# Optimization experiments

Hardware: AMD Instinct MI355X
Metric: run time of the kernel (lower is better)

Reference implementation:

```python
import jax, jax.numpy as jnp
import numpy as np

H, HD = 8, 64  # num_heads, head_dim
EPS = 1e-6

def rmsnorm(x, scale):
    return x * jax.lax.rsqrt(jnp.mean(x * x, axis=-1, keepdims=True) + EPS) * scale

def lecun(key, shape):
    fan_in = shape[0]
    return jax.random.normal(key, shape, dtype=jnp.float32) * (fan_in ** -0.5)

def setup_inputs() -> dict:
    key = jax.random.key(0)
    ks = jax.random.split(key, 12)
    B, S, D = 2, 512, 512
    hidden = H * HD            # 512
    ffn = 4 * D                # 2048
    return {
        "inputs": jax.random.normal(ks[0], (B, S, D), dtype=jnp.float32),
        "mask": jnp.zeros((B, S), dtype=jnp.float32),
        "carry": jnp.zeros((B, H, HD, HD), dtype=jnp.float32),
        "ln1": jnp.ones((D,), dtype=jnp.float32),
        "Wq": lecun(ks[1], (D, hidden)),
        "Wk": lecun(ks[2], (D, hidden)),
        "Wv": lecun(ks[3], (D, hidden)),
        "attn_ln": jnp.ones((hidden,), dtype=jnp.float32),
        "Wo": lecun(ks[4], (hidden, D)),
        "bo": jnp.zeros((D,), dtype=jnp.float32),
        "ln2": jnp.ones((D,), dtype=jnp.float32),
        "Wg": lecun(ks[5], (D, ffn)),
        "Wu": lecun(ks[6], (D, ffn)),
        "Wd": lecun(ks[7], (ffn, D)),
    }

def reference(inputs, mask, carry, ln1, Wq, Wk, Wv, attn_ln, Wo, bo, ln2, Wg, Wu, Wd):
    B, S, D = inputs.shape
    skip = inputs
    x = rmsnorm(inputs, ln1)
    # projections + relu feature map
    q = jax.nn.relu((x @ Wq).reshape(B, S, H, HD))
    k = jax.nn.relu((x @ Wk).reshape(B, S, H, HD))
    v = (x @ Wv).reshape(B, S, H, HD)
    # matrix-valued state update: Bmat_t = v_t k_t^T  [B,S,H,HD,HD]
    Bmat = v[..., :, None] * k[..., None, :]
    # decay: identity, zeroed where mask==1 (episode reset)
    m = mask[:, :, None, None, None]
    A = jnp.broadcast_to(jnp.eye(HD, dtype=x.dtype), Bmat.shape) * (1.0 - m)

    def binop(lhs, rhs):
        a_i, b_i = lhs
        a_j, b_j = rhs
        return jnp.matmul(a_i, a_j), jnp.matmul(b_i, a_j) + b_j

    cum_decay, hidden_states = jax.lax.associative_scan(binop, (A, Bmat), axis=1)
    # fold in incoming carry
    states = jnp.matmul(carry[:, None], cum_decay) + hidden_states  # [B,S,H,HD,HD]
    attn = jnp.matmul(states, q[..., None]).squeeze(-1).reshape(B, S, H * HD)
    attn = rmsnorm(attn, attn_ln)
    y = attn @ Wo + bo
    final_carry = states[:, -1]
    # residual + SwiGLU FFN
    x = y + skip
    skip2 = x
    x = rmsnorm(x, ln2)
    x = (jax.nn.silu(x @ Wg) * (x @ Wu)) @ Wd
    return (final_carry, x + skip2)
```

## Files before the change

kernel.cpp:

```cpp
#include <hip/hip_runtime.h>
#include <math.h>

typedef __bf16 bf16x8 __attribute__((ext_vector_type(8)));
typedef float  f32x4  __attribute__((ext_vector_type(4)));

constexpr int B_=2, S_=512, D_=512, H_=8, HD_=64, FFN_=2048, NC_=8;
constexpr float EPS_=1e-6f;

__device__ __forceinline__ __bf16 f2bf(float f){
    union{float f;unsigned u;}x; x.f=f;
    unsigned r=(x.u+0x7fffu+((x.u>>16)&1u))>>16;
    union{unsigned short s;__bf16 b;}y; y.s=(unsigned short)r; return y.b;
}
__device__ __forceinline__ float bf2f(unsigned short s){
    union{unsigned u;float f;}x; x.u=((unsigned)s)<<16; return x.f;
}
__device__ __forceinline__ void bf8_f32(uint4 p, float* o){
    unsigned w[4]={p.x,p.y,p.z,p.w};
#pragma unroll
    for(int i=0;i<4;i++){ o[2*i]=bf2f((unsigned short)(w[i]&0xffffu)); o[2*i+1]=bf2f((unsigned short)(w[i]>>16)); }
}
__device__ __forceinline__ f32x4 MF(bf16x8 a, bf16x8 b, f32x4 c){
    return __builtin_amdgcn_mfma_f32_16x16x32_bf16(a,b,c,0,0,0);
}
#define GLOAD16(g,l) __builtin_amdgcn_global_load_lds((__attribute__((address_space(1))) const void*)(g),(__attribute__((address_space(3))) void*)(l),16,0,0)

__device__ __forceinline__ void rowsq_atomic(float* accb, int row0, int lane, float p[4]){
#pragma unroll
    for(int r=0;r<4;r++){
        float v = p[r];
        v += __shfl_xor(v, 1, 64);
        v += __shfl_xor(v, 2, 64);
        v += __shfl_xor(v, 4, 64);
        v += __shfl_xor(v, 8, 64);
        if((lane&15)==0) atomicAdd(accb + row0 + r, v);
    }
}

__global__ __launch_bounds__(256) void prep_k(const float* __restrict__ Wg,
    const float* __restrict__ Wu, const float* __restrict__ Wd,
    const float* __restrict__ Wq, const float* __restrict__ Wk,
    const float* __restrict__ Wv, const float* __restrict__ Wo,
    __bf16* __restrict__ WT, const float* __restrict__ inputs,
    float* __restrict__ rs1, float* __restrict__ rs2acc, float* __restrict__ rs3acc){
    __shared__ __bf16 s[64][72];
    int t = blockIdx.x, tid = threadIdx.x;
    if(t >= 1024){
        int row = (t-1024)*4 + (tid>>6), lane = tid&63;
        const float4* p = (const float4*)(inputs + (size_t)row*D_) + lane*2;
        float4 a=p[0], b=p[1];
        float ss = a.x*a.x+a.y*a.y+a.z*a.z+a.w*a.w + b.x*b.x+b.y*b.y+b.z*b.z+b.w*b.w;
        for(int off=32; off>0; off>>=1) ss += __shfl_down(ss, off, 64);
        if(lane==0) rs1[row] = rsqrtf(ss/(float)D_ + EPS_);
        float4 z = {0.f,0.f,0.f,0.f};
        if(t==1024) ((float4*)rs2acc)[tid] = z;
        if(t==1025) ((float4*)rs3acc)[tid] = z;
        return;
    }
    const float* src; __bf16* dst; int K,N,lt;
    if      (t<256){ src=Wg; dst=WT;          K=512;  N=2048; lt=t; }
    else if (t<512){ src=Wu; dst=WT+1048576;  K=512;  N=2048; lt=t-256; }
    else if (t<768){ src=Wd; dst=WT+2097152;  K=2048; N=512;  lt=t-512; }
    else if (t<832){ src=Wq; dst=WT+3145728;  K=512;  N=512;  lt=t-768; }
    else if (t<896){ src=Wk; dst=WT+3407872;  K=512;  N=512;  lt=t-832; }
    else if (t<960){ src=Wv; dst=WT+3670016;  K=512;  N=512;  lt=t-896; }
    else           { src=Wo; dst=WT+3932160;  K=512;  N=512;  lt=t-960; }
    int nt64 = N>>6, tk = lt/nt64, tn = lt%nt64;
    {
        int jk = tid>>2, jn0 = (tid&3)*16;
        const float* p = src + (size_t)(tk*64+jk)*N + tn*64 + jn0;
        float4 a0=((const float4*)p)[0], a1=((const float4*)p)[1],
               a2=((const float4*)p)[2], a3=((const float4*)p)[3];
        bf16x8 w0, w1;
        w0[0]=f2bf(a0.x); w0[1]=f2bf(a0.y); w0[2]=f2bf(a0.z); w0[3]=f2bf(a0.w);
        w0[4]=f2bf(a1.x); w0[5]=f2bf(a1.y); w0[6]=f2bf(a1.z); w0[7]=f2bf(a1.w);
        w1[0]=f2bf(a2.x); w1[1]=f2bf(a2.y); w1[2]=f2bf(a2.z); w1[3]=f2bf(a2.w);
        w1[4]=f2bf(a3.x); w1[5]=f2bf(a3.y); w1[6]=f2bf(a3.z); w1[7]=f2bf(a3.w);
        *(bf16x8*)&s[jk][jn0] = w0; *(bf16x8*)&s[jk][jn0+8] = w1;
    }
    __syncthreads();
    {
        int jn = tid&63, jkq = (tid>>6)*16;
        bf16x8 w0, w1;
#pragma unroll
        for(int j=0;j<8;j++){ w0[j]=s[jkq+j][jn]; w1[j]=s[jkq+8+j][jn]; }
        __bf16* q = dst + (size_t)(tn*64+jn)*K + tk*64 + jkq;
        *(bf16x8*)q = w0; *(bf16x8*)(q+8) = w1;
    }
}

__device__ __forceinline__ void stageB1(const __bf16* __restrict__ Bt, int n0, int K, int kk,
                                        __bf16* sB0, __bf16* sB1, int wave, int lane){
    int row = (wave<<4) + (lane>>2), kq = (lane&3)<<3;
    const __bf16* g = Bt + (size_t)(n0+row)*K + kk + kq;
    GLOAD16(g,      sB0 + (wave<<9));
    GLOAD16(g + 32, sB1 + (wave<<9));
}
struct ARf { float4 a0,a1,a2,a3, g0,g1,g2,g3; };
__device__ __forceinline__ ARf loadA_f32(const float* __restrict__ A, const float* __restrict__ g,
                                         int m0, int K, int kk, int tid){
    int row = tid>>2, kq = (tid&3)<<4;
    const float4* p = (const float4*)(A + (size_t)(m0+row)*K + kk + kq);
    const float4* gp = (const float4*)(g + kk + kq);
    ARf o;
    o.a0=p[0]; o.a1=p[1]; o.a2=p[2]; o.a3=p[3];
    o.g0=gp[0]; o.g1=gp[1]; o.g2=gp[2]; o.g3=gp[3];
    return o;
}
__device__ __forceinline__ void writeA_f32(const ARf& o, float r, __bf16* sA0, __bf16* sA1, int tid){
    int row = tid>>2, kq = (tid&3)<<4;
    bf16x8 w0, w1;
    w0[0]=f2bf(o.a0.x*r*o.g0.x); w0[1]=f2bf(o.a0.y*r*o.g0.y);
    w0[2]=f2bf(o.a0.z*r*o.g0.z); w0[3]=f2bf(o.a0.w*r*o.g0.w);
    w0[4]=f2bf(o.a1.x*r*o.g1.x); w0[5]=f2bf(o.a1.y*r*o.g1.y);
    w0[6]=f2bf(o.a1.z*r*o.g1.z); w0[7]=f2bf(o.a1.w*r*o.g1.w);
    w1[0]=f2bf(o.a2.x*r*o.g2.x); w1[1]=f2bf(o.a2.y*r*o.g2.y);
    w1[2]=f2bf(o.a2.z*r*o.g2.z); w1[3]=f2bf(o.a2.w*r*o.g2.w);
    w1[4]=f2bf(o.a3.x*r*o.g3.x); w1[5]=f2bf(o.a3.y*r*o.g3.y);
    w1[6]=f2bf(o.a3.z*r*o.g3.z); w1[7]=f2bf(o.a3.w*r*o.g3.w);
    __bf16* d = (kq<32) ? (sA0 + row*32 + kq) : (sA1 + row*32 + kq-32);
    *(bf16x8*)d = w0; *(bf16x8*)(d+8) = w1;
}
struct ARb { uint4 p0,p1; float4 g0,g1,g2,g3; };
__device__ __forceinline__ ARb loadA_bf16(const __bf16* __restrict__ A, const float* __restrict__ g,
                                          int m0, int K, int kk, int tid){
    int row = tid>>2, kq = (tid&3)<<4;
    const __bf16* p = A + (size_t)(m0+row)*K + kk + kq;
    const float4* gp = (const float4*)(g + kk + kq);
    ARb o;
    o.p0 = *(const uint4*)p; o.p1 = *(const uint4*)(p+8);
    o.g0=gp[0]; o.g1=gp[1]; o.g2=gp[2]; o.g3=gp[3];
    return o;
}
__device__ __forceinline__ void writeA_bf16(const ARb& o, float r, __bf16* sA0, __bf16* sA1, int tid){
    int row = tid>>2, kq = (tid&3)<<4;
    float v[16]; bf8_f32(o.p0, v); bf8_f32(o.p1, v+8);
    float gf[16] = {o.g0.x,o.g0.y,o.g0.z,o.g0.w, o.g1.x,o.g1.y,o.g1.z,o.g1.w,
                    o.g2.x,o.g2.y,o.g2.z,o.g2.w, o.g3.x,o.g3.y,o.g3.z,o.g3.w};
    bf16x8 w0, w1;
#pragma unroll
    for(int j=0;j<8;j++){ w0[j]=f2bf(v[j]*r*gf[j]); w1[j]=f2bf(v[8+j]*r*gf[8+j]); }
    __bf16* d = (kq<32) ? (sA0 + row*32 + kq) : (sA1 + row*32 + kq-32);
    *(bf16x8*)d = w0; *(bf16x8*)(d+8) = w1;
}
__device__ __forceinline__ void mfma_tile(const __bf16* sA0, const __bf16* sA1,
        const __bf16* sB0, const __bf16* sB1, int wave, int lane, f32x4 acc[4]){
    int ar = (((wave<<4)+(lane&15))<<5) + ((lane>>4)<<3);
    bf16x8 a0 = *(const bf16x8*)(sA0+ar);
    bf16x8 a1 = *(const bf16x8*)(sA1+ar);
#pragma unroll
    for(int nt=0;nt<4;nt++){
        int br = (((nt<<4)+(lane&15))<<5) + ((lane>>4)<<3);
        acc[nt] = MF(a0, *(const bf16x8*)(sB0+br), acc[nt]);
        acc[nt] = MF(a1, *(const bf16x8*)(sB1+br), acc[nt]);
    }
}

__global__ __launch_bounds__(256) void gemm_qkv_k(const float* __restrict__ in,
        const float* __restrict__ rs1, const float* __restrict__ ln1,
        const __bf16* __restrict__ Bt, __bf16* __restrict__ Qb,
        __bf16* __restrict__ Kb, __bf16* __restrict__ Vb){
    __shared__ __bf16 sA0[2][2048], sA1[2][2048], sB0[2][2048], sB1[2][2048];
    int tid=threadIdx.x, wave=tid>>6, lane=tid&63;
    int n0 = blockIdx.x*64, m0 = blockIdx.y*64;
    float r = rs1[m0+(tid>>2)];
    f32x4 acc[4] = {};
    {
        ARf a = loadA_f32(in, ln1, m0, 512, 0, tid);
        stageB1(Bt, n0, 512, 0, sB0[0], sB1[0], wave, lane);
        writeA_f32(a, r, sA0[0], sA1[0], tid);
        __syncthreads();
    }
    int cur = 0;
#pragma unroll
    for(int it=0; it<8; ++it){
        int nxt = cur^1;
        ARf a;
        if(it<7){
            a = loadA_f32(in, ln1, m0, 512, (it+1)*64, tid);
            stageB1(Bt, n0, 512, (it+1)*64, sB0[nxt], sB1[nxt], wave, lane);
        }
        mfma_tile(sA0[cur],sA1[cur],sB0[cur],sB1[cur],wave,lane,acc);
        if(it<7) writeA_f32(a, r, sA0[nxt], sA1[nxt], tid);
        __syncthreads();
        cur = nxt;
    }
    int seg = n0>>9, nc = n0&511;
    __bf16* Out = seg==0 ? Qb : (seg==1 ? Kb : Vb);
    bool rl = seg<2;
    int r0 = (wave<<4) + ((lane>>4)<<2);
#pragma unroll
    for(int nt=0;nt<4;nt++){
        int col = nc + nt*16 + (lane&15);
#pragma unroll
        for(int rr=0;rr<4;rr++){
            float v = acc[nt][rr]; if(rl) v = fmaxf(v,0.f);
            Out[(size_t)(m0+r0+rr)*512 + col] = f2bf(v);
        }
    }
}

__global__ __launch_bounds__(256) void scanA_k(const __bf16* __restrict__ Kb,
        const __bf16* __restrict__ Vb, const float* __restrict__ mask,
        __bf16* __restrict__ MS, float* __restrict__ Pws){
    int bid = blockIdx.x;
    int c = bid&7, h = (bid>>3)&7, b = bid>>6;
    __shared__ __bf16 sKT0[2048], sKT1[2048], sVT0[2048], sVT1[2048];
    __shared__ float scv[64], ssp[64];
    int tid = threadIdx.x, wave = tid>>6, lane = tid&63;
    const __bf16* Kg = Kb + (size_t)(b*512 + c*64)*512 + h*64;
    const __bf16* Vg = Vb + (size_t)(b*512 + c*64)*512 + h*64;
    if(tid<64) scv[tid] = 1.f - mask[b*512 + c*64 + tid];
    __syncthreads();
    if(tid==0){
        float sp = 1.f;
        for(int t=63;t>=0;--t){ ssp[t]=sp; sp*=scv[t]; }
        Pws[bid] = sp;
    }
    __syncthreads();
#pragma unroll
    for(int p=0;p<2;p++){
        int t = (tid>>3) + p*32, i0 = (tid&7)*8;
        uint4 kr = *(const uint4*)(Kg + (size_t)t*512 + i0);
        uint4 vr = *(const uint4*)(Vg + (size_t)t*512 + i0);
        const __bf16* kp = (const __bf16*)&kr;
        const unsigned short* vp = (const unsigned short*)&vr;
        float sp = ssp[t];
        __bf16* kh = p ? sKT1 : sKT0;
        __bf16* vh = p ? sVT1 : sVT0;
#pragma unroll
        for(int j=0;j<8;j++){
            kh[(i0+j)*32 + (t&31)] = kp[j];
            vh[(i0+j)*32 + (t&31)] = f2bf(bf2f(vp[j])*sp);
        }
    }
    __syncthreads();
    f32x4 am[4] = {};
    mfma_tile(sVT0, sVT1, sKT0, sKT1, wave, lane, am);
    __bf16* Mo = MS + (size_t)bid*4096;
    int r0 = (wave<<4) + ((lane>>4)<<2);
#pragma unroll
    for(int nt=0;nt<4;nt++){
        int j = nt*16 + (lane&15);
#pragma unroll
        for(int r=0;r<4;r++) Mo[(size_t)(r0+r)*64 + j] = f2bf(am[nt][r]);
    }
}

__global__ __launch_bounds__(256) void scanC_k(const __bf16* __restrict__ Qb,
        const __bf16* __restrict__ Kb, const __bf16* __restrict__ Vb,
        const float* __restrict__ mask, const __bf16* __restrict__ MS,
        const float* __restrict__ carry, const float* __restrict__ Pws,
        float* __restrict__ carry_out, __bf16* __restrict__ attn,
        float* __restrict__ rs2acc){
    int bid = blockIdx.x;
    int c = bid&7, h = (bid>>3)&7, b = bid>>6;
    int bh = b*H_ + h;
    __shared__ __bf16 sQ0[2048], sQ1[2048], sK0[2048], sK1[2048];
    __shared__ __bf16 sS0[2048], sS1[2048];
    __shared__ __bf16 sVT0[2048], sVT1[2048];
    __shared__ __bf16 sW0[2048], sW1[2048];
    __shared__ float Wtab[64][64];
    __shared__ float scv[64], pp[64];
    int tid = threadIdx.x, wave = tid>>6, lane = tid&63;
    const __bf16* Qg = Qb + (size_t)(b*512 + c*64)*512 + h*64;
    const __bf16* Kg = Kb + (size_t)(b*512 + c*64)*512 + h*64;
    const __bf16* Vg = Vb + (size_t)(b*512 + c*64)*512 + h*64;

    stageB1(Qg, 0, 512, 0, sQ0, sQ1, wave, lane);
    stageB1(Kg, 0, 512, 0, sK0, sK1, wave, lane);
    if(tid<64) scv[tid] = 1.f - mask[b*512 + c*64 + tid];
#pragma unroll
    for(int p=0;p<2;p++){
        int u = (tid>>3) + p*32, i0 = (tid&7)*8;
        uint4 vr = *(const uint4*)(Vg + (size_t)u*512 + i0);
        const __bf16* vp = (const __bf16*)&vr;
        __bf16* vh = p ? sVT1 : sVT0;
#pragma unroll
        for(int j=0;j<8;j++) vh[(i0+j)*32 + (u&31)] = vp[j];
    }
    {
        int i = tid>>2, j0 = (tid&3)*16;
        float s[16];
        const float4* c4 = (const float4*)(carry + (size_t)bh*4096 + i*64 + j0);
        float4 s4[4] = {c4[0],c4[1],c4[2],c4[3]};
        float* sp = (float*)s4;
#pragma unroll
        for(int j=0;j<16;j++) s[j]=sp[j];
        for(int cc=0; cc<c; ++cc){
            float P = Pws[bh*8+cc];
            const __bf16* mp = MS + ((size_t)bh*8+cc)*4096 + i*64 + j0;
            float mv[16]; bf8_f32(*(const uint4*)mp, mv); bf8_f32(*(const uint4*)(mp+8), mv+8);
#pragma unroll
            for(int j=0;j<16;j++) s[j] = s[j]*P + mv[j];
        }
        bf16x8 w0, w1;
#pragma unroll
        for(int j=0;j<8;j++){ w0[j]=f2bf(s[j]); w1[j]=f2bf(s[8+j]); }
        __bf16* d = (j0<32) ? (sS0 + i*32 + j0) : (sS1 + i*32 + j0-32);
        *(bf16x8*)d = w0; *(bf16x8*)(d+8) = w1;
        if(c==7){
            float P = Pws[bh*8+7];
            const __bf16* mp = MS + ((size_t)bh*8+7)*4096 + i*64 + j0;
            float mv[16]; bf8_f32(*(const uint4*)mp, mv); bf8_f32(*(const uint4*)(mp+8), mv+8);
            float4 o4[4];
            float* ov = (float*)o4;
#pragma unroll
            for(int j=0;j<16;j++) ov[j] = s[j]*P + mv[j];
            float4* co = (float4*)(carry_out + (size_t)bh*4096 + i*64 + j0);
            co[0]=o4[0]; co[1]=o4[1]; co[2]=o4[2]; co[3]=o4[3];
        }
    }
    __syncthreads();
    if(tid<64){
        int u = tid; float w = 1.f;
        for(int t=0;t<64;t++){
            if(t>u) w *= scv[t];
            Wtab[u][t] = (t<u) ? 0.f : w;
        }
    }
    if(tid==64){
        float p=1.f;
        for(int t=0;t<64;t++){ p*=scv[t]; pp[t]=p; }
    }
    f32x4 sc[4] = {};
    mfma_tile(sK0, sK1, sQ0, sQ1, wave, lane, sc);
    __syncthreads();
    {
        int u0 = (wave<<4) + ((lane>>4)<<2);
#pragma unroll
        for(int nt=0;nt<4;nt++){
            int t = nt*16 + (lane&15);
#pragma unroll
            for(int r=0;r<4;r++){
                int u = u0 + r;
                float v = sc[nt][r] * Wtab[u][t];
                ((u<32) ? sW0 : sW1)[t*32 + (u&31)] = f2bf(v);
            }
        }
    }
    __syncthreads();
    f32x4 aI[4] = {}, aX[4] = {};
    mfma_tile(sW0, sW1, sVT0, sVT1, wave, lane, aI);
    mfma_tile(sQ0, sQ1, sS0, sS1, wave, lane, aX);
    int t0 = (wave<<4) + ((lane>>4)<<2);
    float psum[4] = {0.f,0.f,0.f,0.f};
#pragma unroll
    for(int nt=0;nt<4;nt++){
        int i = nt*16 + (lane&15);
#pragma unroll
        for(int r=0;r<4;r++){
            int t = t0 + r;
            float o = aI[nt][r] + aX[nt][r]*pp[t];
            attn[(size_t)(b*512 + c*64 + t)*512 + h*64 + i] = f2bf(o);
            psum[r] += o*o;
        }
    }
    rowsq_atomic(rs2acc, b*512 + c*64 + t0, lane, psum);
}

__global__ __launch_bounds__(256) void gemm_wo_k(const __bf16* __restrict__ attn,
        const float* __restrict__ rs2acc, const float* __restrict__ aln,
        const __bf16* __restrict__ Bt, const float* __restrict__ bo,
        const float* __restrict__ skip, float* __restrict__ outx,
        __bf16* __restrict__ X1, float* __restrict__ rs3acc){
    __shared__ __bf16 sA0[2][2048], sA1[2][2048], sB0[2][2048], sB1[2][2048];
    int tid=threadIdx.x, wave=tid>>6, lane=tid&63;
    int n0 = blockIdx.x*64, m0 = blockIdx.y*64;
    float r = rsqrtf(rs2acc[m0+(tid>>2)]*(1.f/(float)D_) + EPS_);
    f32x4 acc[4] = {};
    {
        ARb a = loadA_bf16(attn, aln, m0, 512, 0, tid);
        stageB1(Bt, n0, 512, 0, sB0[0], sB1[0], wave, lane);
        writeA_bf16(a, r, sA0[0], sA1[0], tid);
        __syncthreads();
    }
    int cur = 0;
#pragma unroll
    for(int it=0; it<8; ++it){
        int nxt = cur^1;
        ARb a;
        if(it<7){
            a = loadA_bf16(attn, aln, m0, 512, (it+1)*64, tid);
            stageB1(Bt, n0, 512, (it+1)*64, sB0[nxt], sB1[nxt], wave, lane);
        }
        mfma_tile(sA0[cur],sA1[cur],sB0[cur],sB1[cur],wave,lane,acc);
        if(it<7) writeA_bf16(a, r, sA0[nxt], sA1[nxt], tid);
        __syncthreads();
        cur = nxt;
    }
    int r0 = (wave<<4) + ((lane>>4)<<2);
    float psum[4] = {0.f,0.f,0.f,0.f};
#pragma unroll
    for(int nt=0;nt<4;nt++){
        int col = n0 + nt*16 + (lane&15);
#pragma unroll
        for(int rr=0;rr<4;rr++){
            int row = m0+r0+rr;
            float v = acc[nt][rr] + bo[col] + skip[(size_t)row*512+col];
            outx[(size_t)row*512+col] = v;
            X1[(size_t)row*512+col] = f2bf(v);
            psum[rr] += v*v;
        }
    }
    rowsq_atomic(rs3acc, m0+r0, lane, psum);
}

__global__ __launch_bounds__(256) void gemm_dual_k(const __bf16* __restrict__ X1,
        const float* __restrict__ rs3acc, const float* __restrict__ ln2,
        const __bf16* __restrict__ Gt, const __bf16* __restrict__ Ut,
        __bf16* __restrict__ Hb){
    __shared__ __bf16 sA0[2][2048], sA1[2][2048];
    __shared__ __bf16 sG0[2][2048], sG1[2][2048], sU0[2][2048], sU1[2][2048];
    int tid=threadIdx.x, wave=tid>>6, lane=tid&63;
    int n0 = blockIdx.x*64, m0 = blockIdx.y*64;
    float r = rsqrtf(rs3acc[m0+(tid>>2)]*(1.f/(float)D_) + EPS_);
    f32x4 ag[4] = {}, au[4] = {};
    {
        ARb a = loadA_bf16(X1, ln2, m0, 512, 0, tid);
        stageB1(Gt, n0, 512, 0, sG0[0], sG1[0], wave, lane);
        stageB1(Ut, n0, 512, 0, sU0[0], sU1[0], wave, lane);
        writeA_bf16(a, r, sA0[0], sA1[0], tid);
        __syncthreads();
    }
    int cur = 0;
#pragma unroll
    for(int it=0; it<8; ++it){
        int nxt = cur^1;
        ARb a;
        if(it<7){
            a = loadA_bf16(X1, ln2, m0, 512, (it+1)*64, tid);
            stageB1(Gt, n0, 512, (it+1)*64, sG0[nxt], sG1[nxt], wave, lane);
            stageB1(Ut, n0, 512, (it+1)*64, sU0[nxt], sU1[nxt], wave, lane);
        }
        {
            int ar = (((wave<<4)+(lane&15))<<5) + ((lane>>4)<<3);
            bf16x8 a0 = *(const bf16x8*)(sA0[cur]+ar);
            bf16x8 a1 = *(const bf16x8*)(sA1[cur]+ar);
#pragma unroll
            for(int nt=0;nt<4;nt++){
                int br = (((nt<<4)+(lane&15))<<5) + ((lane>>4)<<3);
                ag[nt] = MF(a0, *(const bf16x8*)(sG0[cur]+br), ag[nt]);
                ag[nt] = MF(a1, *(const bf16x8*)(sG1[cur]+br), ag[nt]);
                au[nt] = MF(a0, *(const bf16x8*)(sU0[cur]+br), au[nt]);
                au[nt] = MF(a1, *(const bf16x8*)(sU1[cur]+br), au[nt]);
            }
        }
        if(it<7) writeA_bf16(a, r, sA0[nxt], sA1[nxt], tid);
        __syncthreads();
        cur = nxt;
    }
    int r0 = (wave<<4) + ((lane>>4)<<2);
#pragma unroll
    for(int nt=0;nt<4;nt++){
        int col = n0 + nt*16 + (lane&15);
#pragma unroll
        for(int rr=0;rr<4;rr++){
            float gv = ag[nt][rr], uv = au[nt][rr];
            float hv = (gv / (1.f + __expf(-gv))) * uv;
            Hb[(size_t)(m0+r0+rr)*FFN_ + col] = f2bf(hv);
        }
    }
}

__global__ __launch_bounds__(256) void gemm_wd_k(const __bf16* __restrict__ Hb,
        const __bf16* __restrict__ Bt, float* __restrict__ outx){
    __shared__ __bf16 sA0[2][2048], sA1[2][2048], sB0[2][2048], sB1[2][2048];
    int tid=threadIdx.x, wave=tid>>6, lane=tid&63;
    int n0 = blockIdx.x*64, m0 = blockIdx.y*64, ks = blockIdx.z*512;
    f32x4 acc[4] = {};
    int row = (wave<<4) + (lane>>2), kq = (lane&3)<<3;
    {
        stageB1(Bt, n0, FFN_, ks, sB0[0], sB1[0], wave, lane);
        const __bf16* g = Hb + (size_t)(m0+row)*FFN_ + ks + kq;
        GLOAD16(g,      sA0[0] + (wave<<9));
        GLOAD16(g + 32, sA1[0] + (wave<<9));
        __syncthreads();
    }
    int cur = 0;
#pragma unroll
    for(int it=0; it<8; ++it){
        int nxt = cur^1;
        if(it<7){
            int kk = ks + (it+1)*64;
            stageB1(Bt, n0, FFN_, kk, sB0[nxt], sB1[nxt], wave, lane);
            const __bf16* g = Hb + (size_t)(m0+row)*FFN_ + kk + kq;
            GLOAD16(g,      sA0[nxt] + (wave<<9));
            GLOAD16(g + 32, sA1[nxt] + (wave<<9));
        }
        mfma_tile(sA0[cur],sA1[cur],sB0[cur],sB1[cur],wave,lane,acc);
        __syncthreads();
        cur = nxt;
    }
    int r0 = (wave<<4) + ((lane>>4)<<2);
#pragma unroll
    for(int nt=0;nt<4;nt++){
        int col = n0 + nt*16 + (lane&15);
#pragma unroll
        for(int r=0;r<4;r++)
            atomicAdd(&outx[(size_t)(m0+r0+r)*512 + col], acc[nt][r]);
    }
}

extern "C" void kernel_launch(void* const* d_in, const int* in_sizes, int n_in,
                              void* d_out, int out_size, void* d_ws, size_t ws_size,
                              hipStream_t stream) {
    const float* inputs  = (const float*)d_in[0];
    const float* mask    = (const float*)d_in[1];
    const float* carry   = (const float*)d_in[2];
    const float* ln1     = (const float*)d_in[3];
    const float* Wq      = (const float*)d_in[4];
    const float* Wk      = (const float*)d_in[5];
    const float* Wv      = (const float*)d_in[6];
    const float* attn_ln = (const float*)d_in[7];
    const float* Wo      = (const float*)d_in[8];
    const float* bo      = (const float*)d_in[9];
    const float* ln2     = (const float*)d_in[10];
    const float* Wg      = (const float*)d_in[11];
    const float* Wu      = (const float*)d_in[12];
    const float* Wd      = (const float*)d_in[13];

    float* out_carry = (float*)d_out;
    float* out_x     = (float*)d_out + 65536;

    __bf16* wb = (__bf16*)d_ws;
    float*  wf = (float*)d_ws;
    __bf16* WgT   = wb;
    __bf16* WuT   = wb + 1048576;
    __bf16* WdT   = wb + 2097152;
    __bf16* WqkvT = wb + 3145728;
    __bf16* WoT   = wb + 3932160;
    __bf16* Qb    = wb + 4194304;
    __bf16* Kb    = wb + 4718592;
    __bf16* Vb    = wb + 5242880;
    __bf16* Hb    = wb + 3145728;
    __bf16* MS    = wb + 5767168;
    float*  Pws   = wf + 3145728;
    float*  rs1   = wf + 3145856;
    float*  rs2a  = wf + 3146880;
    float*  rs3a  = wf + 3147904;

    prep_k<<<dim3(1280), dim3(256), 0, stream>>>(Wg,Wu,Wd,Wq,Wk,Wv,Wo, wb, inputs, rs1, rs2a, rs3a);
    gemm_qkv_k<<<dim3(24,16), dim3(256), 0, stream>>>(inputs, rs1, ln1, WqkvT, Qb, Kb, Vb);
    scanA_k<<<dim3(128), dim3(256), 0, stream>>>(Kb, Vb, mask, MS, Pws);
    scanC_k<<<dim3(128), dim3(256), 0, stream>>>(Qb, Kb, Vb, mask, MS, carry, Pws, out_carry, Qb, rs2a);
    gemm_wo_k<<<dim3(8,16), dim3(256), 0, stream>>>(Qb, rs2a, attn_ln, WoT, bo, inputs, out_x, Vb, rs3a);
    gemm_dual_k<<<dim3(32,16), dim3(256), 0, stream>>>(Vb, rs3a, ln2, WgT, WuT, Hb);
    gemm_wd_k<<<dim3(8,16,4), dim3(256), 0, stream>>>(Hb, WdT, out_x);
}
```

Baseline: 161.7 us.

## Stage GEMM epilogues through LDS for coalesced stores; drop split-K in Wd GEMM

Several kernels (QKV, scanC, Wo, dual SwiGLU) now write their bf16 output tiles into shared memory first and then store them with 16-byte coalesced row writes, instead of scattered 2-byte stores. The scan kernels' shared buffers are merged into contiguous arrays. The Wd GEMM drops its 4-way split-K with atomics and runs the full K=2048 loop per block, finishing with a plain read-add-write. That removes atomic traffic but cuts the Wd grid to 128 blocks, each with a 4x longer serial loop.

Measured after the change: 175.9 us. 1.09x slower.

```diff
diff --git a/kernel.cpp b/kernel.cpp
--- a/kernel.cpp
+++ b/kernel.cpp
@@ -188,15 +188,22 @@
     int seg = n0>>9, nc = n0&511;
     __bf16* Out = seg==0 ? Qb : (seg==1 ? Kb : Vb);
     bool rl = seg<2;
+    __bf16* tile = &sA0[0][0];
     int r0 = (wave<<4) + ((lane>>4)<<2);
 #pragma unroll
     for(int nt=0;nt<4;nt++){
-        int col = nc + nt*16 + (lane&15);
+        int col = nt*16 + (lane&15);
 #pragma unroll
         for(int rr=0;rr<4;rr++){
             float v = acc[nt][rr]; if(rl) v = fmaxf(v,0.f);
-            Out[(size_t)(m0+r0+rr)*512 + col] = f2bf(v);
-        }
+            tile[(r0+rr)*64 + col] = f2bf(v);
+        }
+    }
+    __syncthreads();
+#pragma unroll
+    for(int p=0;p<2;p++){
+        int row = (tid>>3) + p*32, c0 = (tid&7)*8;
+        *(uint4*)(Out + (size_t)(m0+row)*512 + nc + c0) = *(const uint4*)&tile[row*64 + c0];
     }
 }
 
@@ -205,7 +212,7 @@
         __bf16* __restrict__ MS, float* __restrict__ Pws){
     int bid = blockIdx.x;
     int c = bid&7, h = (bid>>3)&7, b = bid>>6;
-    __shared__ __bf16 sKT0[2048], sKT1[2048], sVT0[2048], sVT1[2048];
+    __shared__ __bf16 sKT[4096], sVT[4096];
     __shared__ float scv[64], ssp[64];
     int tid = threadIdx.x, wave = tid>>6, lane = tid&63;
     const __bf16* Kg = Kb + (size_t)(b*512 + c*64)*512 + h*64;
@@ -226,8 +233,8 @@
         const __bf16* kp = (const __bf16*)&kr;
         const unsigned short* vp = (const unsigned short*)&vr;
         float sp = ssp[t];
-        __bf16* kh = p ? sKT1 : sKT0;
-        __bf16* vh = p ? sVT1 : sVT0;
+        __bf16* kh = (t<32) ? sKT : sKT+2048;
+        __bf16* vh = (t<32) ? sVT : sVT+2048;
 #pragma unroll
         for(int j=0;j<8;j++){
             kh[(i0+j)*32 + (t&31)] = kp[j];
@@ -236,7 +243,7 @@
     }
     __syncthreads();
     f32x4 am[4] = {};
-    mfma_tile(sVT0, sVT1, sKT0, sKT1, wave, lane, am);
+    mfma_tile(sVT, sVT+2048, sKT, sKT+2048, wave, lane, am);
     __bf16* Mo = MS + (size_t)bid*4096;
     int r0 = (wave<<4) + ((lane>>4)<<2);
 #pragma unroll
@@ -256,10 +263,7 @@
     int bid = blockIdx.x;
     int c = bid&7, h = (bid>>3)&7, b = bid>>6;
     int bh = b*H_ + h;
-    __shared__ __bf16 sQ0[2048], sQ1[2048], sK0[2048], sK1[2048];
-    __shared__ __bf16 sS0[2048], sS1[2048];
-    __shared__ __bf16 sVT0[2048], sVT1[2048];
-    __shared__ __bf16 sW0[2048], sW1[2048];
+    __shared__ __bf16 sQ[4096], sK[4096], sS[4096], sVT[4096], sW[4096];
     __shared__ float Wtab[64][64];
     __shared__ float scv[64], pp[64];
     int tid = threadIdx.x, wave = tid>>6, lane = tid&63;
@@ -267,15 +271,15 @@
     const __bf16* Kg = Kb + (size_t)(b*512 + c*64)*512 + h*64;
     const __bf16* Vg = Vb + (size_t)(b*512 + c*64)*512 + h*64;
 
-    stageB1(Qg, 0, 512, 0, sQ0, sQ1, wave, lane);
-    stageB1(Kg, 0, 512, 0, sK0, sK1, wave, lane);
+    stageB1(Qg, 0, 512, 0, sQ, sQ+2048, wave, lane);
+    stageB1(Kg, 0, 512, 0, sK, sK+2048, wave, lane);
     if(tid<64) scv[tid] = 1.f - mask[b*512 + c*64 + tid];
 #pragma unroll
     for(int p=0;p<2;p++){
         int u = (tid>>3) + p*32, i0 = (tid&7)*8;
         uint4 vr = *(const uint4*)(Vg + (size_t)u*512 + i0);
         const __bf16* vp = (const __bf16*)&vr;
-        __bf16* vh = p ? sVT1 : sVT0;
+        __bf16* vh = (u<32) ? sVT : sVT+2048;
 #pragma unroll
         for(int j=0;j<8;j++) vh[(i0+j)*32 + (u&31)] = vp[j];
     }
@@ -297,7 +301,7 @@
         bf16x8 w0, w1;
 #pragma unroll
         for(int j=0;j<8;j++){ w0[j]=f2bf(s[j]); w1[j]=f2bf(s[8+j]); }
-        __bf16* d = (j0<32) ? (sS0 + i*32 + j0) : (sS1 + i*32 + j0-32);
+        __bf16* d = (j0<32) ? (sS + i*32 + j0) : (sS+2048 + i*32 + j0-32);
         *(bf16x8*)d = w0; *(bf16x8*)(d+8) = w1;
         if(c==7){
             float P = Pws[bh*8+7];
@@ -324,7 +328,7 @@
         for(int t=0;t<64;t++){ p*=scv[t]; pp[t]=p; }
     }
     f32x4 sc[4] = {};
-    mfma_tile(sK0, sK1, sQ0, sQ1, wave, lane, sc);
+    mfma_tile(sK, sK+2048, sQ, sQ+2048, wave, lane, sc);
     __syncthreads();
     {
         int u0 = (wave<<4) + ((lane>>4)<<2);
@@ -335,28 +339,43 @@
             for(int r=0;r<4;r++){
                 int u = u0 + r;
                 float v = sc[nt][r] * Wtab[u][t];
-                ((u<32) ? sW0 : sW1)[t*32 + (u&31)] = f2bf(v);
+                ((u<32)? sW : sW+2048)[t*32 + (u&31)] = f2bf(v);
             }
         }
     }
     __syncthreads();
     f32x4 aI[4] = {}, aX[4] = {};
-    mfma_tile(sW0, sW1, sVT0, sVT1, wave, lane, aI);
-    mfma_tile(sQ0, sQ1, sS0, sS1, wave, lane, aX);
+    mfma_tile(sW, sW+2048, sVT, sVT+2048, wave, lane, aI);
+    mfma_tile(sQ, sQ+2048, sS, sS+2048, wave, lane, aX);
     int t0 = (wave<<4) + ((lane>>4)<<2);
+    float attv[4][4];
     float psum[4] = {0.f,0.f,0.f,0.f};
 #pragma unroll
     for(int nt=0;nt<4;nt++){
-        int i = nt*16 + (lane&15);
 #pragma unroll
         for(int r=0;r<4;r++){
             int t = t0 + r;
             float o = aI[nt][r] + aX[nt][r]*pp[t];
-            attn[(size_t)(b*512 + c*64 + t)*512 + h*64 + i] = f2bf(o);
+            attv[nt][r] = o;
             psum[r] += o*o;
         }
     }
     rowsq_atomic(rs2acc, b*512 + c*64 + t0, lane, psum);
+    __syncthreads();
+    __bf16* tile = sW;
+#pragma unroll
+    for(int nt=0;nt<4;nt++){
+        int i = nt*16 + (lane&15);
+#pragma unroll
+        for(int r=0;r<4;r++) tile[(t0+r)*64 + i] = f2bf(attv[nt][r]);
+    }
+    __syncthreads();
+#pragma unroll
+    for(int p=0;p<2;p++){
+        int row = (tid>>3) + p*32, c0 = (tid&7)*8;
+        *(uint4*)(attn + (size_t)(b*512 + c*64 + row)*512 + h*64 + c0) =
+            *(const uint4*)&tile[row*64 + c0];
+    }
 }
 
 __global__ __launch_bounds__(256) void gemm_wo_k(const __bf16* __restrict__ attn,
@@ -391,6 +410,7 @@
     }
     int r0 = (wave<<4) + ((lane>>4)<<2);
     float psum[4] = {0.f,0.f,0.f,0.f};
+    __bf16* tile = &sA0[0][0];
 #pragma unroll
     for(int nt=0;nt<4;nt++){
         int col = n0 + nt*16 + (lane&15);
@@ -399,11 +419,17 @@
             int row = m0+r0+rr;
             float v = acc[nt][rr] + bo[col] + skip[(size_t)row*512+col];
             outx[(size_t)row*512+col] = v;
-            X1[(size_t)row*512+col] = f2bf(v);
+            tile[(r0+rr)*64 + nt*16 + (lane&15)] = f2bf(v);
             psum[rr] += v*v;
         }
     }
     rowsq_atomic(rs3acc, m0+r0, lane, psum);
+    __syncthreads();
+#pragma unroll
+    for(int p=0;p<2;p++){
+        int row = (tid>>3) + p*32, c0 = (tid&7)*8;
+        *(uint4*)(X1 + (size_t)(m0+row)*512 + n0 + c0) = *(const uint4*)&tile[row*64 + c0];
+    }
 }
 
 __global__ __launch_bounds__(256) void gemm_dual_k(const __bf16* __restrict__ X1,
@@ -451,15 +477,22 @@
         cur = nxt;
     }
     int r0 = (wave<<4) + ((lane>>4)<<2);
-#pragma unroll
-    for(int nt=0;nt<4;nt++){
-        int col = n0 + nt*16 + (lane&15);
+    __bf16* tile = &sA0[0][0];
+#pragma unroll
+    for(int nt=0;nt<4;nt++){
+        int col = nt*16 + (lane&15);
 #pragma unroll
         for(int rr=0;rr<4;rr++){
             float gv = ag[nt][rr], uv = au[nt][rr];
             float hv = (gv / (1.f + __expf(-gv))) * uv;
-            Hb[(size_t)(m0+r0+rr)*FFN_ + col] = f2bf(hv);
-        }
+            tile[(r0+rr)*64 + col] = f2bf(hv);
+        }
+    }
+    __syncthreads();
+#pragma unroll
+    for(int p=0;p<2;p++){
+        int row = (tid>>3) + p*32, c0 = (tid&7)*8;
+        *(uint4*)(Hb + (size_t)(m0+row)*FFN_ + n0 + c0) = *(const uint4*)&tile[row*64 + c0];
     }
 }
 
@@ -467,22 +500,21 @@
         const __bf16* __restrict__ Bt, float* __restrict__ outx){
     __shared__ __bf16 sA0[2][2048], sA1[2][2048], sB0[2][2048], sB1[2][2048];
     int tid=threadIdx.x, wave=tid>>6, lane=tid&63;
-    int n0 = blockIdx.x*64, m0 = blockIdx.y*64, ks = blockIdx.z*512;
+    int n0 = blockIdx.x*64, m0 = blockIdx.y*64;
     f32x4 acc[4] = {};
     int row = (wave<<4) + (lane>>2), kq = (lane&3)<<3;
     {
-        stageB1(Bt, n0, FFN_, ks, sB0[0], sB1[0], wave, lane);
-        const __bf16* g = Hb + (size_t)(m0+row)*FFN_ + ks + kq;
+        stageB1(Bt, n0, FFN_, 0, sB0[0], sB1[0], wave, lane);
+        const __bf16* g = Hb + (size_t)(m0+row)*FFN_ + kq;
         GLOAD16(g,      sA0[0] + (wave<<9));
         GLOAD16(g + 32, sA1[0] + (wave<<9));
         __syncthreads();
     }
     int cur = 0;
-#pragma unroll
-    for(int it=0; it<8; ++it){
+    for(int it=0; it<32; ++it){
         int nxt = cur^1;
-        if(it<7){
-            int kk = ks + (it+1)*64;
+        if(it<31){
+            int kk = (it+1)*64;
             stageB1(Bt, n0, FFN_, kk, sB0[nxt], sB1[nxt], wave, lane);
             const __bf16* g = Hb + (size_t)(m0+row)*FFN_ + kk + kq;
             GLOAD16(g,      sA0[nxt] + (wave<<9));
@@ -497,8 +529,10 @@
     for(int nt=0;nt<4;nt++){
         int col = n0 + nt*16 + (lane&15);
 #pragma unroll
-        for(int r=0;r<4;r++)
-            atomicAdd(&outx[(size_t)(m0+r0+r)*512 + col], acc[nt][r]);
+        for(int rr=0;rr<4;rr++){
+            size_t idx = (size_t)(m0+r0+rr)*512 + col;
+            outx[idx] = outx[idx] + acc[nt][rr];
+        }
     }
 }
 
@@ -546,5 +580,5 @@
     scanC_k<<<dim3(128), dim3(256), 0, stream>>>(Qb, Kb, Vb, mask, MS, carry, Pws, out_carry, Qb, rs2a);
     gemm_wo_k<<<dim3(8,16), dim3(256), 0, stream>>>(Qb, rs2a, attn_ln, WoT, bo, inputs, out_x, Vb, rs3a);
     gemm_dual_k<<<dim3(32,16), dim3(256), 0, stream>>>(Vb, rs3a, ln2, WgT, WuT, Hb);
-    gemm_wd_k<<<dim3(8,16,4), dim3(256), 0, stream>>>(Hb, WdT, out_x);
-}
+    gemm_wd_k<<<dim3(8,16), dim3(256), 0, stream>>>(Hb, WdT, out_x);
+}
```
